# Kernel optimization log

Measured on AMD Instinct MI355X. Metric: run time of the kernel, lower is better.

## Reference

```python
import jax, jax.numpy as jnp
import numpy as np

B, T, D_MODEL = 2, 2048, 2048
NH, NKV, DH = 16, 4, 128
N_REP = NH // NKV
NV = 256  # n_vision_tokens
THETA = 10000.0
NEG = -1e9


def setup_inputs() -> dict:
    key = jax.random.key(0)
    ks = jax.random.split(key, 5)
    x = jax.random.normal(ks[0], (B, T, D_MODEL), jnp.float32)
    # rope_freqs = exp(i * t * theta^{-2j/D}) represented as cos/sin, shape [T, DH//2]
    inv = 1.0 / (THETA ** (np.arange(0, DH, 2, dtype=np.float64) / DH))
    ang = np.outer(np.arange(T, dtype=np.float64), inv)
    cos = jnp.asarray(np.cos(ang), jnp.float32)
    sin = jnp.asarray(np.sin(ang), jnp.float32)
    sc = 0.02
    wq = jax.random.normal(ks[1], (D_MODEL, NH * DH), jnp.float32) * sc
    wk = jax.random.normal(ks[2], (D_MODEL, NKV * DH), jnp.float32) * sc
    wv = jax.random.normal(ks[3], (D_MODEL, NKV * DH), jnp.float32) * sc
    wo = jax.random.normal(ks[4], (NH * DH, D_MODEL), jnp.float32) * sc
    return {"x": x, "cos": cos, "sin": sin, "wq": wq, "wk": wk, "wv": wv,
            "wo": wo, "n_vision_tokens": NV}


def _rope(t, cos, sin):
    # t: [B,H,L,D]; pairs (even=real, odd=imag); cos/sin: [L, D//2]
    a = t[..., 0::2]
    b = t[..., 1::2]
    c = cos[None, None]
    s = sin[None, None]
    ra = a * c - b * s
    rb = a * s + b * c
    return jnp.stack([ra, rb], axis=-1).reshape(t.shape)


def reference(x, cos, sin, wq, wk, wv, wo, n_vision_tokens):
    Bx, Tx, _ = x.shape
    nv = int(n_vision_tokens)
    tl = Tx - nv  # text length

    q = (x @ wq).reshape(Bx, Tx, NH, DH).transpose(0, 2, 1, 3)   # [B,NH,T,DH]
    k = (x @ wk).reshape(Bx, Tx, NKV, DH).transpose(0, 2, 1, 3)  # [B,NKV,T,DH]
    v = (x @ wv).reshape(Bx, Tx, NKV, DH).transpose(0, 2, 1, 3)

    # RoPE only on the text portion (vision tokens keep raw q/k)
    c, s = cos[:tl], sin[:tl]
    q = jnp.concatenate([q[:, :, :nv], _rope(q[:, :, nv:], c, s)], axis=2)
    k = jnp.concatenate([k[:, :, :nv], _rope(k[:, :, nv:], c, s)], axis=2)

    new_kv_cache = (k, v)

    # GQA: repeat_interleave KV heads
    k = jnp.repeat(k, N_REP, axis=1)
    v = jnp.repeat(v, N_REP, axis=1)

    attn = jnp.einsum('bhqd,bhkd->bhqk', q, k) / jnp.sqrt(jnp.float32(DH))

    # hybrid mask: vision rows/cols fully visible; text-text strictly causal
    text_mask = jnp.triu(jnp.ones((tl, tl), bool), k=1)
    mask = jnp.zeros((Tx, Tx), bool).at[nv:, nv:].set(text_mask)
    attn = jnp.where(mask[None, None], NEG, attn)

    attn = jax.nn.softmax(attn, axis=-1)
    out = jnp.einsum('bhqk,bhkd->bhqd', attn, v)
    out = out.transpose(0, 2, 1, 3).reshape(Bx, Tx, NH * DH) @ wo
    return out, new_kv_cache
```

## Files before the change

### kernel.cpp

```cpp
#include <hip/hip_runtime.h>
#include <hip/hip_bf16.h>

#define BB 2
#define TT 2048
#define DMODEL 2048
#define NH 16
#define NKV 4
#define DH 128
#define NV 256
#define TL (TT - NV)
#define NQKV 3072

typedef __bf16  bf16x8  __attribute__((ext_vector_type(8)));
typedef float   float4v __attribute__((ext_vector_type(4)));
typedef short   short8  __attribute__((ext_vector_type(8)));
typedef unsigned short ushort;

__device__ __forceinline__ float bf2f(ushort u) {
    union { float f; unsigned i; } c; c.i = ((unsigned)u) << 16; return c.f;
}
__device__ __forceinline__ ushort f2bf(float f) {
    union { float f; unsigned i; } c; c.f = f;
    unsigned r = c.i + 0x7fff + ((c.i >> 16) & 1);
    return (ushort)(r >> 16);
}
__device__ __forceinline__ unsigned cvtpk(float a, float b) {
    unsigned r;
    asm("v_cvt_pk_bf16_f32 %0, %1, %2" : "=v"(r) : "v"(a), "v"(b));
    return r;
}

#define GLDS16(g, l) __builtin_amdgcn_global_load_lds( \
    (__attribute__((address_space(1))) void*)(g), \
    (__attribute__((address_space(3))) void*)(l), 16, 0, 0)

__global__ __launch_bounds__(256) void convert_x(
    const float* __restrict__ x, ushort* __restrict__ xbf)
{
    size_t i = ((size_t)blockIdx.x * 256 + threadIdx.x) * 8;
    float4v f0 = *(const float4v*)&x[i];
    float4v f1 = *(const float4v*)&x[i + 4];
    short8 h;
    h[0] = (short)f2bf(f0[0]); h[1] = (short)f2bf(f0[1]);
    h[2] = (short)f2bf(f0[2]); h[3] = (short)f2bf(f0[3]);
    h[4] = (short)f2bf(f1[0]); h[5] = (short)f2bf(f1[1]);
    h[6] = (short)f2bf(f1[2]); h[7] = (short)f2bf(f1[3]);
    *(short8*)&xbf[i] = h;
}

__global__ __launch_bounds__(256) void wtrans_all(
    const float* __restrict__ wq, const float* __restrict__ wk,
    const float* __restrict__ wv, ushort* __restrict__ wT)
{
    __shared__ ushort st[64][72];
    int n0 = blockIdx.x * 64, k0 = blockIdx.y * 64;
    const float* w; int N, nn;
    if (n0 < 2048)      { w = wq; N = 2048; nn = n0; }
    else if (n0 < 2560) { w = wk; N = 512;  nn = n0 - 2048; }
    else                { w = wv; N = 512;  nn = n0 - 2560; }
    int r  = threadIdx.x >> 2;
    int c0 = (threadIdx.x & 3) * 16;
    #pragma unroll
    for (int j = 0; j < 16; j += 4) {
        float4v f = *(const float4v*)&w[(size_t)(k0 + r) * N + nn + c0 + j];
        st[c0 + j + 0][r] = f2bf(f[0]);
        st[c0 + j + 1][r] = f2bf(f[1]);
        st[c0 + j + 2][r] = f2bf(f[2]);
        st[c0 + j + 3][r] = f2bf(f[3]);
    }
    __syncthreads();
    ushort* dst = &wT[(size_t)(n0 + r) * DMODEL + k0];
    *(short8*)&dst[c0]     = *(short8*)&st[r][c0];
    *(short8*)&dst[c0 + 8] = *(short8*)&st[r][c0 + 8];
}

__global__ __launch_bounds__(256) void wtrans_wo(
    const float* __restrict__ w, ushort* __restrict__ qkv)
{
    __shared__ ushort st[64][72];
    int n0 = blockIdx.x * 64, k0 = blockIdx.y * 64;
    int r  = threadIdx.x >> 2;
    int c0 = (threadIdx.x & 3) * 16;
    #pragma unroll
    for (int j = 0; j < 16; j += 4) {
        float4v f = *(const float4v*)&w[(size_t)(k0 + r) * DMODEL + n0 + c0 + j];
        st[c0 + j + 0][r] = f2bf(f[0]);
        st[c0 + j + 1][r] = f2bf(f[1]);
        st[c0 + j + 2][r] = f2bf(f[2]);
        st[c0 + j + 3][r] = f2bf(f[3]);
    }
    __syncthreads();
    ushort* dst = qkv + ((size_t)(2 * (n0 + r) + (k0 >> 10))) * NQKV + 2048 + (k0 & 1023);
    *(short8*)&dst[c0]     = *(short8*)&st[r][c0];
    *(short8*)&dst[c0 + 8] = *(short8*)&st[r][c0 + 8];
}

#define RQ_BLOCKS 14336
#define RK_BLOCKS 4096
__global__ __launch_bounds__(256) void postproc(
    ushort* __restrict__ qkv,
    const float* __restrict__ cosp, const float* __restrict__ sinp,
    float* __restrict__ kout, float* __restrict__ vout,
    ushort* __restrict__ kbf, ushort* __restrict__ vbfT)
{
    __shared__ ushort st[64][72];
    int bid = blockIdx.x;
    if (bid < RQ_BLOCKS) {
        int b   = bid / (RQ_BLOCKS / 2);
        int idx = (bid % (RQ_BLOCKS / 2)) * 256 + threadIdx.x;
        int i  = idx & 63;
        int h  = (idx >> 6) & 15;
        int tr = idx >> 10;
        int t  = NV + tr;
        size_t off = ((size_t)(b * TT + t)) * NQKV + h * DH + 2 * i;
        unsigned pk = *(const unsigned*)&qkv[off];
        float a  = bf2f((ushort)(pk & 0xffff));
        float bb = bf2f((ushort)(pk >> 16));
        float c  = cosp[tr * 64 + i];
        float s  = sinp[tr * 64 + i];
        *(unsigned*)&qkv[off] = cvtpk(a * c - bb * s, a * s + bb * c);
        return;
    }
    bid -= RQ_BLOCKS;
    if (bid < RK_BLOCKS) {
        int idx = bid * 256 + threadIdx.x;
        int i  = idx & 63;
        int kh = (idx >> 6) & 3;
        int t  = (idx >> 8) & 2047;
        int b  = idx >> 19;
        size_t row = ((size_t)(b * TT + t)) * NQKV;
        size_t dst = ((size_t)((b * NKV + kh) * TT + t)) * DH + 2 * i;
        unsigned pk = *(const unsigned*)&qkv[row + 2048 + kh * DH + 2 * i];
        float ka = bf2f((ushort)(pk & 0xffff));
        float kb = bf2f((ushort)(pk >> 16));
        if (t >= NV) {
            int pos = t - NV;
            float c = cosp[pos * 64 + i];
            float s = sinp[pos * 64 + i];
            float ra = ka * c - kb * s;
            float rb = ka * s + kb * c;
            ka = ra; kb = rb;
        }
        kout[dst]     = ka;
        kout[dst + 1] = kb;
        *(unsigned*)&kbf[dst] = cvtpk(ka, kb);
        unsigned pv = *(const unsigned*)&qkv[row + 2560 + kh * DH + 2 * i];
        vout[dst]     = bf2f((ushort)(pv & 0xffff));
        vout[dst + 1] = bf2f((ushort)(pv >> 16));
        return;
    }
    bid -= RK_BLOCKS;
    {
        int bx = bid & 31, by = (bid >> 5) & 1, bk = bid >> 6;
        int t0 = bx * 64, d0 = by * 64;
        int b = bk >> 2, kh = bk & 3;
        int r  = threadIdx.x >> 2;
        int c0 = (threadIdx.x & 3) * 16;
        const ushort* src = qkv + ((size_t)(b * TT + t0 + r)) * NQKV + 2560 + kh * DH + d0;
        short8 a0 = *(const short8*)&src[c0];
        short8 a1 = *(const short8*)&src[c0 + 8];
        #pragma unroll
        for (int j = 0; j < 8; j++) {
            st[c0 + j][r]     = (ushort)a0[j];
            st[c0 + 8 + j][r] = (ushort)a1[j];
        }
        __syncthreads();
        ushort* dst = vbfT + ((size_t)(bk * DH + d0 + r)) * TT + t0;
        *(short8*)&dst[c0]     = *(short8*)&st[r][c0];
        *(short8*)&dst[c0 + 8] = *(short8*)&st[r][c0 + 8];
    }
}

__global__ __launch_bounds__(256) void gemm_lds(
    const ushort* __restrict__ A, int lda,
    const ushort* __restrict__ BT,
    ushort* __restrict__ C, int ldc, int K)
{
    __shared__ ushort As[2][128 * 32];
    __shared__ ushort Bs[2][128 * 32];

    int tid = threadIdx.x;
    int wave = tid >> 6, lane = tid & 63, quad = lane >> 4, l16 = lane & 15;

    int nwg = gridDim.x * gridDim.y;
    int bid = blockIdx.x + gridDim.x * blockIdx.y;
    int cpx = nwg >> 3;
    int swz = (bid & 7) * cpx + (bid >> 3);
    int bx = swz % gridDim.x, by = swz / gridDim.x;
    int m0 = by * 128, n0 = bx * 128;
    int wr = (wave >> 1) * 64, wc = (wave & 1) * 64;

    int srow = tid >> 2, scol = (tid & 3) * 8;
    const ushort* ag = A  + (size_t)(m0 + srow) * lda + scol;
    const ushort* bg = BT + (size_t)(n0 + srow) * K   + scol;
    int lo0 = (wave * 16) * 32;
    int lo1 = (64 + wave * 16) * 32;

    float4v acc[4][4];
    for (int i = 0; i < 4; i++)
        for (int j = 0; j < 4; j++)
            acc[i][j] = (float4v){0.f, 0.f, 0.f, 0.f};

    auto stage = [&](int buf, int k0) {
        GLDS16(ag + k0,                    As[buf] + lo0);
        GLDS16(ag + (size_t)64 * lda + k0, As[buf] + lo1);
        GLDS16(bg + k0,                    Bs[buf] + lo0);
        GLDS16(bg + (size_t)64 * K + k0,   Bs[buf] + lo1);
    };

    stage(0, 0);
    int it = 0;
    for (int k0 = 0; k0 < K; k0 += 32, ++it) {
        int cur = it & 1;
        __syncthreads();
        if (k0 + 32 < K) stage(cur ^ 1, k0 + 32);

        bf16x8 af[4], bfr[4];
        #pragma unroll
        for (int i = 0; i < 4; i++) af[i] = *(const bf16x8*)&As[cur][(wr + i * 16 + l16) * 32 + quad * 8];
        #pragma unroll
        for (int j = 0; j < 4; j++) bfr[j] = *(const bf16x8*)&Bs[cur][(wc + j * 16 + l16) * 32 + quad * 8];
        #pragma unroll
        for (int i = 0; i < 4; i++)
            #pragma unroll
            for (int j = 0; j < 4; j++)
                acc[i][j] = __builtin_amdgcn_mfma_f32_16x16x32_bf16(af[i], bfr[j], acc[i][j], 0, 0, 0);
    }

    #pragma unroll
    for (int i = 0; i < 4; i++)
        #pragma unroll
        for (int j = 0; j < 4; j++)
            #pragma unroll
            for (int r = 0; r < 4; r++) {
                int row = m0 + wr + i * 16 + quad * 4 + r;
                int col = n0 + wc + j * 16 + l16;
                C[(size_t)row * ldc + col] = f2bf(acc[i][j][r]);
            }
}

__global__ __launch_bounds__(256) void gemm_out(
    const ushort* __restrict__ A,
    const ushort* __restrict__ Bc,
    float* __restrict__ C)
{
    __shared__ ushort As[2][128 * 32];
    __shared__ ushort Bs[2][128 * 32];

    int tid = threadIdx.x;
    int wave = tid >> 6, lane = tid & 63, quad = lane >> 4, l16 = lane & 15;

    int nwg = gridDim.x * gridDim.y;
    int bid = blockIdx.x + gridDim.x * blockIdx.y;
    int cpx = nwg >> 3;
    int swz = (bid & 7) * cpx + (bid >> 3);
    int bx = swz % gridDim.x, by = swz / gridDim.x;
    int m0 = by * 128, n0 = bx * 128;
    int wr = (wave >> 1) * 64, wc = (wave & 1) * 64;

    int srow = tid >> 2, scol = (tid & 3) * 8;
    const ushort* ag = A  + (size_t)(m0 + srow) * NQKV + scol;
    const ushort* bg = Bc + (size_t)(n0 + srow) * 6144 + scol;
    int lo0 = (wave * 16) * 32;
    int lo1 = (64 + wave * 16) * 32;

    float4v acc[4][4];
    for (int i = 0; i < 4; i++)
        for (int j = 0; j < 4; j++)
            acc[i][j] = (float4v){0.f, 0.f, 0.f, 0.f};

    auto stage = [&](int buf, int k0) {
        int koff = ((k0 >> 10) * NQKV) + (k0 & 1023);
        GLDS16(ag + k0,                       As[buf] + lo0);
        GLDS16(ag + (size_t)64 * NQKV + k0,   As[buf] + lo1);
        GLDS16(bg + koff,                     Bs[buf] + lo0);
        GLDS16(bg + (size_t)64 * 6144 + koff, Bs[buf] + lo1);
    };

    stage(0, 0);
    int it = 0;
    for (int k0 = 0; k0 < 2048; k0 += 32, ++it) {
        int cur = it & 1;
        __syncthreads();
        if (k0 + 32 < 2048) stage(cur ^ 1, k0 + 32);

        bf16x8 af[4], bfr[4];
        #pragma unroll
        for (int i = 0; i < 4; i++) af[i] = *(const bf16x8*)&As[cur][(wr + i * 16 + l16) * 32 + quad * 8];
        #pragma unroll
        for (int j = 0; j < 4; j++) bfr[j] = *(const bf16x8*)&Bs[cur][(wc + j * 16 + l16) * 32 + quad * 8];
        #pragma unroll
        for (int i = 0; i < 4; i++)
            #pragma unroll
            for (int j = 0; j < 4; j++)
                acc[i][j] = __builtin_amdgcn_mfma_f32_16x16x32_bf16(af[i], bfr[j], acc[i][j], 0, 0, 0);
    }

    #pragma unroll
    for (int i = 0; i < 4; i++)
        #pragma unroll
        for (int j = 0; j < 4; j++)
            #pragma unroll
            for (int r = 0; r < 4; r++) {
                int row = m0 + wr + i * 16 + quad * 4 + r;
                int col = n0 + wc + j * 16 + l16;
                C[(size_t)row * DMODEL + col] = acc[i][j][r];
            }
}

__global__ __launch_bounds__(256, 2) void attn_kernel(
    ushort* qkv,
    const ushort* __restrict__ kbf, const ushort* __restrict__ vbfT)
{
    __shared__ ushort shm[32768];

    int tid = threadIdx.x;
    int wave = tid >> 6, lane = tid & 63, quad = lane >> 4, l16 = lane & 15;
    int hy = blockIdx.x;
    int qx = blockIdx.y;
    int qt = (qx < 4) ? qx : (35 - qx);
    int b  = blockIdx.z;
    int h0 = hy * 2;
    int kh = hy >> 1;
    int q0 = qt * 64;

    int srow = tid >> 2, scol = (tid & 3) * 8;

    ushort* qbase0 = qkv + ((size_t)(b * TT) + q0) * NQKV + h0 * DH;
    ushort* qbase1 = qbase0 + DH;
    #pragma unroll
    for (int dk = 0; dk < 4; dk++) {
        GLDS16(qbase0 + (size_t)srow * NQKV + dk * 32 + scol, shm + dk * 2048 + wave * 512);
        GLDS16(qbase1 + (size_t)srow * NQKV + dk * 32 + scol, shm + 16384 + dk * 2048 + wave * 512);
    }
    __syncthreads();
    bf16x8 qf0[4], qf1[4];
    #pragma unroll
    for (int dk = 0; dk < 4; dk++) {
        qf0[dk] = *(const bf16x8*)&shm[dk * 2048 + (wave * 16 + l16) * 32 + quad * 8];
        qf1[dk] = *(const bf16x8*)&shm[16384 + dk * 2048 + (wave * 16 + l16) * 32 + quad * 8];
    }
    __syncthreads();

    float4v O0[8], O1[8];
    #pragma unroll
    for (int i = 0; i < 8; i++) {
        O0[i] = (float4v){0.f, 0.f, 0.f, 0.f};
        O1[i] = (float4v){0.f, 0.f, 0.f, 0.f};
    }
    float m0r = -1e30f, l0r = 0.f;
    float m1r = -1e30f, l1r = 0.f;

    int nkt = (q0 < NV) ? (TT / 64) : (qt + 1);
    const float scale = 0.08838834764831845f;
    const float THRR  = 90.50966799f;
    int qg = q0 + wave * 16 + l16;

    const ushort* kb2 = kbf  + ((size_t)(b * NKV + kh)) * TT * DH;
    const ushort* vb2 = vbfT + ((size_t)(b * NKV + kh)) * DH * TT;

    int sl0 = ((lane & 16) << 1) + l16;
    int sl1 = sl0 + 16;
    bool hi = lane >= 32;

    auto stage = [&](int buf, int kt) {
        ushort* Kb = shm + buf * 16384;
        ushort* Vb = Kb + 8192;
        int k0 = kt * 64;
        #pragma unroll
        for (int dk = 0; dk < 4; dk++)
            GLDS16(kb2 + (size_t)(k0 + srow) * DH + dk * 32 + scol, Kb + dk * 2048 + wave * 512);
        #pragma unroll
        for (int kk = 0; kk < 2; kk++)
            #pragma unroll
            for (int p = 0; p < 2; p++)
                GLDS16(vb2 + (size_t)(p * 64 + srow) * TT + k0 + kk * 32 + scol,
                       Vb + kk * 4096 + (p * 64 + wave * 16) * 32);
    };

    stage(0, 0);

    for (int kt = 0; kt < nkt; kt++) {
        int cur = kt & 1;
        __syncthreads();
        if (kt + 1 < nkt)
            stage(cur ^ 1, kt + 1);

        const ushort* Kc = shm + cur * 16384;
        const ushort* Vc = Kc + 8192;
        int k0 = kt * 64;

        float4v s0[4], s1[4];
        __builtin_amdgcn_s_setprio(1);
        #pragma unroll
        for (int t2i = 0; t2i < 4; t2i++) {
            float4v a0 = (float4v){0.f, 0.f, 0.f, 0.f};
            float4v a1 = (float4v){0.f, 0.f, 0.f, 0.f};
            #pragma unroll
            for (int dk = 0; dk < 4; dk++) {
                bf16x8 af = *(const bf16x8*)&Kc[dk * 2048 + (t2i * 16 + l16) * 32 + quad * 8];
                a0 = __builtin_amdgcn_mfma_f32_16x16x32_bf16(af, qf0[dk], a0, 0, 0, 0);
                a1 = __builtin_amdgcn_mfma_f32_16x16x32_bf16(af, qf1[dk], a1, 0, 0, 0);
            }
            s0[t2i] = a0; s1[t2i] = a1;
        }
        __builtin_amdgcn_s_setprio(0);

        if ((q0 >= NV) && (kt == qt)) {
            #pragma unroll
            for (int t2i = 0; t2i < 4; t2i++)
                #pragma unroll
                for (int i = 0; i < 4; i++)
                    if (k0 + t2i * 16 + quad * 4 + i > qg) {
                        s0[t2i][i] = -1e9f;
                        s1[t2i][i] = -1e9f;
                    }
        }

        float mx0 = -1e30f, mx1 = -1e30f;
        #pragma unroll
        for (int t2i = 0; t2i < 4; t2i++)
            #pragma unroll
            for (int i = 0; i < 4; i++) {
                mx0 = fmaxf(mx0, s0[t2i][i]);
                mx1 = fmaxf(mx1, s1[t2i][i]);
            }
        mx0 = fmaxf(mx0, __shfl_xor(mx0, 16, 64));
        mx0 = fmaxf(mx0, __shfl_xor(mx0, 32, 64));
        mx1 = fmaxf(mx1, __shfl_xor(mx1, 16, 64));
        mx1 = fmaxf(mx1, __shfl_xor(mx1, 32, 64));

        bool skip0 = __all(mx0 <= m0r + THRR);
        bool skip1 = __all(mx1 <= m1r + THRR);
        float mn0 = fmaxf(m0r, mx0), mn1 = fmaxf(m1r, mx1);
        float mref0 = skip0 ? m0r : mn0;
        float mref1 = skip1 ? m1r : mn1;
        float nb0 = -mref0 * scale;
        float nb1 = -mref1 * scale;

        float ss0 = 0.f, ss1 = 0.f;
        #pragma unroll
        for (int t2i = 0; t2i < 4; t2i++)
            #pragma unroll
            for (int i = 0; i < 4; i++) {
                float p0 = __expf(__builtin_fmaf(s0[t2i][i], scale, nb0)); s0[t2i][i] = p0; ss0 += p0;
                float p1 = __expf(__builtin_fmaf(s1[t2i][i], scale, nb1)); s1[t2i][i] = p1; ss1 += p1;
            }
        ss0 += __shfl_xor(ss0, 16, 64); ss0 += __shfl_xor(ss0, 32, 64);
        ss1 += __shfl_xor(ss1, 16, 64); ss1 += __shfl_xor(ss1, 32, 64);

        if (!skip0) {
            float al0 = __expf((m0r - mn0) * scale);
            #pragma unroll
            for (int dt = 0; dt < 8; dt++)
                #pragma unroll
                for (int i = 0; i < 4; i++) O0[dt][i] *= al0;
            l0r *= al0;
            m0r = mn0;
        }
        l0r += ss0;
        if (!skip1) {
            float al1 = __expf((m1r - mn1) * scale);
            #pragma unroll
            for (int dt = 0; dt < 8; dt++)
                #pragma unroll
                for (int i = 0; i < 4; i++) O1[dt][i] *= al1;
            l1r *= al1;
            m1r = mn1;
        }
        l1r += ss1;

        unsigned p01a[4], p23a[4], p01b[4], p23b[4];
        #pragma unroll
        for (int t2i = 0; t2i < 4; t2i++) {
            p01a[t2i] = cvtpk(s0[t2i][0], s0[t2i][1]);
            p23a[t2i] = cvtpk(s0[t2i][2], s0[t2i][3]);
            p01b[t2i] = cvtpk(s1[t2i][0], s1[t2i][1]);
            p23b[t2i] = cvtpk(s1[t2i][2], s1[t2i][3]);
        }

        #pragma unroll
        for (int kk = 0; kk < 2; kk++) {
            int ta = 2 * kk, tb = 2 * kk + 1;
            union { unsigned u[4]; bf16x8 v; } pf0, pf1;
            {
                unsigned A0 = __shfl(p01a[ta], sl0, 64), B0 = __shfl(p01a[tb], sl0, 64);
                unsigned A1 = __shfl(p23a[ta], sl0, 64), B1 = __shfl(p23a[tb], sl0, 64);
                unsigned A2 = __shfl(p01a[ta], sl1, 64), B2 = __shfl(p01a[tb], sl1, 64);
                unsigned A3 = __shfl(p23a[ta], sl1, 64), B3 = __shfl(p23a[tb], sl1, 64);
                pf0.u[0] = hi ? B0 : A0;
                pf0.u[1] = hi ? B1 : A1;
                pf0.u[2] = hi ? B2 : A2;
                pf0.u[3] = hi ? B3 : A3;
            }
            {
                unsigned A0 = __shfl(p01b[ta], sl0, 64), B0 = __shfl(p01b[tb], sl0, 64);
                unsigned A1 = __shfl(p23b[ta], sl0, 64), B1 = __shfl(p23b[tb], sl0, 64);
                unsigned A2 = __shfl(p01b[ta], sl1, 64), B2 = __shfl(p01b[tb], sl1, 64);
                unsigned A3 = __shfl(p23b[ta], sl1, 64), B3 = __shfl(p23b[tb], sl1, 64);
                pf1.u[0] = hi ? B0 : A0;
                pf1.u[1] = hi ? B1 : A1;
                pf1.u[2] = hi ? B2 : A2;
                pf1.u[3] = hi ? B3 : A3;
            }
            __builtin_amdgcn_s_setprio(1);
            #pragma unroll
            for (int dt = 0; dt < 8; dt++) {
                bf16x8 vf = *(const bf16x8*)&Vc[kk * 4096 + (dt * 16 + l16) * 32 + quad * 8];
                O0[dt] = __builtin_amdgcn_mfma_f32_16x16x32_bf16(vf, pf0.v, O0[dt], 0, 0, 0);
                O1[dt] = __builtin_amdgcn_mfma_f32_16x16x32_bf16(vf, pf1.v, O1[dt], 0, 0, 0);
            }
            __builtin_amdgcn_s_setprio(0);
        }
    }

    float rinv0 = 1.f / l0r, rinv1 = 1.f / l1r;
    size_t orow = (size_t)(wave * 16 + l16) * NQKV;
    #pragma unroll
    for (int dt = 0; dt < 8; dt++)
        #pragma unroll
        for (int i = 0; i < 4; i += 2) {
            unsigned pk0 = cvtpk(O0[dt][i] * rinv0, O0[dt][i + 1] * rinv0);
            unsigned pk1 = cvtpk(O1[dt][i] * rinv1, O1[dt][i + 1] * rinv1);
            *(unsigned*)&qbase0[orow + dt * 16 + quad * 4 + i] = pk0;
            *(unsigned*)&qbase1[orow + dt * 16 + quad * 4 + i] = pk1;
        }
}

extern "C" void kernel_launch(void* const* d_in, const int* in_sizes, int n_in,
                              void* d_out, int out_size, void* d_ws, size_t ws_size,
                              hipStream_t stream) {
    const float* x    = (const float*)d_in[0];
    const float* cosp = (const float*)d_in[1];
    const float* sinp = (const float*)d_in[2];
    const float* wq   = (const float*)d_in[3];
    const float* wk   = (const float*)d_in[4];
    const float* wv   = (const float*)d_in[5];
    const float* wo   = (const float*)d_in[6];

    float* out  = (float*)d_out;
    float* kout = out + (size_t)BB * TT * DMODEL;
    float* vout = kout + (size_t)BB * NKV * TT * DH;

    ushort* sc    = (ushort*)d_out;
    ushort* wqkvT = sc;
    ushort* xbf   = sc + (size_t)NQKV * DMODEL;
    ushort* kbf   = sc + (size_t)NQKV * DMODEL;
    ushort* vbfT  = kbf + (size_t)BB * NKV * TT * DH;

    ushort* qkv = (ushort*)d_ws;

    const int M = BB * TT;

    convert_x<<<dim3((size_t)M * DMODEL / 2048), 256, 0, stream>>>(x, xbf);
    wtrans_all<<<dim3(NQKV / 64, DMODEL / 64), 256, 0, stream>>>(wq, wk, wv, wqkvT);

    gemm_lds<<<dim3(NQKV / 128, M / 128), 256, 0, stream>>>(
        xbf, DMODEL, wqkvT, qkv, NQKV, DMODEL);

    postproc<<<dim3(RQ_BLOCKS + RK_BLOCKS + 512), 256, 0, stream>>>(
        qkv, cosp, sinp, kout, vout, kbf, vbfT);

    wtrans_wo<<<dim3(DMODEL / 64, DMODEL / 64), 256, 0, stream>>>(wo, qkv);

    attn_kernel<<<dim3(NH / 2, TT / 64, BB), 256, 0, stream>>>(qkv, kbf, vbfT);

    gemm_out<<<dim3(DMODEL / 128, M / 128), 256, 0, stream>>>(qkv, qkv + 2048, out);
}
```

Baseline: 355.3 us.

## Split long attention query tiles across KV ranges and merge partial results

Replaces the one-block-per-query-tile attention grid with a 51-entry job table. The longest tiles (vision rows and late causal rows) are split into two KV ranges, each writing a normalized partial output plus its running max and sum. A new combine kernel merges the two halves with softmax rescaling. The aim is to balance work across blocks and shorten the tail of the attention launch, at the cost of an extra kernel launch and extra global traffic for the partials, which reuse scratch space in the output buffer.

```diff
diff --git a/kernel.cpp b/kernel.cpp
--- a/kernel.cpp
+++ b/kernel.cpp
@@ -33,6 +33,29 @@
 #define GLDS16(g, l) __builtin_amdgcn_global_load_lds( \
     (__attribute__((address_space(1))) void*)(g), \
     (__attribute__((address_space(3))) void*)(l), 16, 0, 0)
+
+#define NJOB 51
+#define NSLOT 19
+__device__ const short J_QT[NJOB] = {
+    16,  0, 0, 1, 1, 2, 2, 3, 3, 31, 31, 30, 15,
+    30, 29, 29, 28, 14, 28, 27, 27, 26, 13, 26, 25, 25, 24, 12,
+    24, 23, 23, 22, 11, 22, 21, 21, 20, 10, 20, 19, 19, 18,  9,
+    18, 17, 17,  8,  7,  6,  5,  4 };
+__device__ const short J_K0[NJOB] = {
+     0,  0,16, 0,16, 0,16, 0,16,  0, 16,  0,  0,
+    16,  0,15, 0,  0, 15,  0, 14,  0,  0, 14,  0, 13,  0,  0,
+    13,  0,12, 0,  0, 12,  0, 11,  0,  0, 11,  0, 10,  0,  0,
+    10,  0, 9, 0,  0,  0,  0,  0 };
+__device__ const short J_K1[NJOB] = {
+    17, 16,32,16,32,16,32,16,32, 16, 32, 16, 16,
+    31, 15,30,15, 15, 29, 14, 28, 14, 14, 27, 13, 26, 13, 13,
+    25, 12,24,12, 12, 23, 11, 22, 11, 11, 21, 10, 20, 10, 10,
+    19,  9,18, 9,  8,  7,  6,  5 };
+__device__ const short J_PH[NJOB] = {
+   255,  0, 1, 2, 3, 4, 5, 6, 7, 36, 37, 34,255,
+    35, 32,33,30,255, 31, 28, 29, 26,255, 27, 24, 25, 22,255,
+    23, 20,21,18,255, 19, 16, 17, 14,255, 15, 12, 13, 10,255,
+    11,  8, 9,255,255,255,255,255 };
 
 __global__ __launch_bounds__(256) void convert_x(
     const float* __restrict__ x, ushort* __restrict__ xbf)
@@ -310,16 +333,20 @@
 
 __global__ __launch_bounds__(256, 2) void attn_kernel(
     ushort* qkv,
-    const ushort* __restrict__ kbf, const ushort* __restrict__ vbfT)
+    const ushort* __restrict__ kbf, const ushort* __restrict__ vbfT,
+    ushort* __restrict__ pO, float* __restrict__ ml)
 {
     __shared__ ushort shm[32768];
 
     int tid = threadIdx.x;
     int wave = tid >> 6, lane = tid & 63, quad = lane >> 4, l16 = lane & 15;
     int hy = blockIdx.x;
-    int qx = blockIdx.y;
-    int qt = (qx < 4) ? qx : (35 - qx);
+    int job = blockIdx.y;
     int b  = blockIdx.z;
+    int qt  = J_QT[job];
+    int kt0 = J_K0[job];
+    int kt1 = J_K1[job];
+    int ph  = J_PH[job];
     int h0 = hy * 2;
     int kh = hy >> 1;
     int q0 = qt * 64;
@@ -351,7 +378,6 @@
     float m0r = -1e30f, l0r = 0.f;
     float m1r = -1e30f, l1r = 0.f;
 
-    int nkt = (q0 < NV) ? (TT / 64) : (qt + 1);
     const float scale = 0.08838834764831845f;
     const float THRR  = 90.50966799f;
     int qg = q0 + wave * 16 + l16;
@@ -378,12 +404,12 @@
                        Vb + kk * 4096 + (p * 64 + wave * 16) * 32);
     };
 
-    stage(0, 0);
-
-    for (int kt = 0; kt < nkt; kt++) {
-        int cur = kt & 1;
+    stage(0, kt0);
+
+    for (int kt = kt0; kt < kt1; kt++) {
+        int cur = (kt - kt0) & 1;
         __syncthreads();
-        if (kt + 1 < nkt)
+        if (kt + 1 < kt1)
             stage(cur ^ 1, kt + 1);
 
         const ushort* Kc = shm + cur * 16384;
@@ -515,16 +541,77 @@
     }
 
     float rinv0 = 1.f / l0r, rinv1 = 1.f / l1r;
-    size_t orow = (size_t)(wave * 16 + l16) * NQKV;
-    #pragma unroll
-    for (int dt = 0; dt < 8; dt++)
-        #pragma unroll
-        for (int i = 0; i < 4; i += 2) {
-            unsigned pk0 = cvtpk(O0[dt][i] * rinv0, O0[dt][i + 1] * rinv0);
-            unsigned pk1 = cvtpk(O1[dt][i] * rinv1, O1[dt][i + 1] * rinv1);
-            *(unsigned*)&qbase0[orow + dt * 16 + quad * 4 + i] = pk0;
-            *(unsigned*)&qbase1[orow + dt * 16 + quad * 4 + i] = pk1;
-        }
+    int qrow = wave * 16 + l16;
+    if (ph == 255 || (ph & 1)) {
+        size_t orow = (size_t)qrow * NQKV;
+        #pragma unroll
+        for (int dt = 0; dt < 8; dt++)
+            #pragma unroll
+            for (int i = 0; i < 4; i += 2) {
+                unsigned pk0 = cvtpk(O0[dt][i] * rinv0, O0[dt][i + 1] * rinv0);
+                unsigned pk1 = cvtpk(O1[dt][i] * rinv1, O1[dt][i + 1] * rinv1);
+                *(unsigned*)&qbase0[orow + dt * 16 + quad * 4 + i] = pk0;
+                *(unsigned*)&qbase1[orow + dt * 16 + quad * 4 + i] = pk1;
+            }
+    } else {
+        int g = ((b * 8 + hy) * NSLOT) + (ph >> 1);
+        ushort* pb = pO + (size_t)g * 16384 + qrow * 256;
+        #pragma unroll
+        for (int dt = 0; dt < 8; dt++)
+            #pragma unroll
+            for (int i = 0; i < 4; i += 2) {
+                int d = dt * 16 + quad * 4 + i;
+                *(unsigned*)&pb[d]       = cvtpk(O0[dt][i] * rinv0, O0[dt][i + 1] * rinv0);
+                *(unsigned*)&pb[128 + d] = cvtpk(O1[dt][i] * rinv1, O1[dt][i + 1] * rinv1);
+            }
+    }
+    if (ph != 255 && quad == 0) {
+        int g = ((b * 8 + hy) * NSLOT) + (ph >> 1);
+        int half = ph & 1;
+        float* mlb = ml + (size_t)g * 512 + half * 256 + qrow * 2;
+        mlb[0]   = m0r;  mlb[1]   = l0r;
+        mlb[128] = m1r;  mlb[129] = l1r;
+    }
+}
+
+__global__ __launch_bounds__(256) void combine_split(
+    ushort* __restrict__ qkv, const ushort* __restrict__ pO,
+    const float* __restrict__ ml)
+{
+    int g = blockIdx.x;
+    int slice = g / NSLOT, local = g % NSLOT;
+    int b = slice >> 3, hy = slice & 7;
+    int qt = (local < 4) ? local : (13 + local);
+    int h0 = hy * 2;
+    int q0 = qt * 64;
+
+    int t = threadIdx.x;
+    int r = t >> 2, seg = t & 3;
+    int head = seg >> 1;
+    const float scale = 0.08838834764831845f;
+
+    const float* mlg = ml + (size_t)g * 512;
+    float m0 = mlg[0 * 256 + head * 128 + r * 2];
+    float l0 = mlg[0 * 256 + head * 128 + r * 2 + 1];
+    float m1 = mlg[1 * 256 + head * 128 + r * 2];
+    float l1 = mlg[1 * 256 + head * 128 + r * 2 + 1];
+    float mm = fmaxf(m0, m1);
+    float w0 = __expf((m0 - mm) * scale) * l0;
+    float w1 = __expf((m1 - mm) * scale) * l1;
+    float inv = 1.f / (w0 + w1);
+    float a0 = w0 * inv, a1 = w1 * inv;
+
+    const ushort* p = pO + (size_t)g * 16384 + r * 256 + seg * 64;
+    ushort* q = qkv + ((size_t)(b * TT + q0 + r)) * NQKV + (h0 + head) * DH + (seg & 1) * 64;
+
+    #pragma unroll
+    for (int j = 0; j < 64; j += 2) {
+        unsigned u0 = *(const unsigned*)&p[j];
+        unsigned u1 = *(const unsigned*)&q[j];
+        float lo = bf2f((ushort)(u0 & 0xffff)) * a0 + bf2f((ushort)(u1 & 0xffff)) * a1;
+        float hi2 = bf2f((ushort)(u0 >> 16)) * a0 + bf2f((ushort)(u1 >> 16)) * a1;
+        *(unsigned*)&q[j] = cvtpk(lo, hi2);
+    }
 }
 
 extern "C" void kernel_launch(void* const* d_in, const int* in_sizes, int n_in,
@@ -547,6 +634,8 @@
     ushort* xbf   = sc + (size_t)NQKV * DMODEL;
     ushort* kbf   = sc + (size_t)NQKV * DMODEL;
     ushort* vbfT  = kbf + (size_t)BB * NKV * TT * DH;
+    ushort* pO    = sc;
+    float*  ml    = (float*)(sc + 15000000);
 
     ushort* qkv = (ushort*)d_ws;
 
@@ -563,7 +652,9 @@
 
     wtrans_wo<<<dim3(DMODEL / 64, DMODEL / 64), 256, 0, stream>>>(wo, qkv);
 
-    attn_kernel<<<dim3(NH / 2, TT / 64, BB), 256, 0, stream>>>(qkv, kbf, vbfT);
+    attn_kernel<<<dim3(NH / 2, NJOB, BB), 256, 0, stream>>>(qkv, kbf, vbfT, pO, ml);
+
+    combine_split<<<dim3(16 * NSLOT), 256, 0, stream>>>(qkv, pO, ml);
 
     gemm_out<<<dim3(DMODEL / 128, M / 128), 256, 0, stream>>>(qkv, qkv + 2048, out);
 }
```

New measurement: 348.3 us. 2.0% less time.
